# Kernel optimization log

Measured on AMD Instinct MI355X. Metric: run time of the kernel, lower is better.

Reference implementation:

```python
import jax, jax.numpy as jnp
import numpy as np

B = 65536
L, R, D, C = 4, 8, 16, 4
M = D * C          # 64 = d_s2*C
D_S1C = 32         # d_s1*C
OUT = 8


def setup_inputs() -> dict:
    key = jax.random.key(0)
    ks = jax.random.split(key, 16)
    inp = {
        'x': jax.random.uniform(ks[0], (B, 8), dtype=jnp.float32),
        'H': jax.random.normal(ks[1], (B, L, R, D, C), dtype=jnp.float32) * 0.1,
        # VNNILinear / Linear params (not quantized by default -> plain F.linear)
        'W_bit': jax.random.normal(ks[2], (D_S1C, 8), dtype=jnp.float32) * 0.02,
        'b_bit': jnp.zeros((D_S1C,), jnp.float32),
        'W_bridge': jax.random.normal(ks[3], (M, D_S1C), dtype=jnp.float32) * 0.02,
        'W_read': jax.random.normal(ks[4], (OUT, R * M), dtype=jnp.float32) * 0.02,
        'b_read': jnp.zeros((OUT,), jnp.float32),
        # Governor
        'W_sh': jax.random.normal(ks[5], (64, M), dtype=jnp.float32) * 0.02,
        'b_sh': jnp.zeros((64,), jnp.float32),
        'W_eng': jax.random.normal(ks[6], (1, 64), dtype=jnp.float32) * 0.02,
        'b_eng': jnp.zeros((1,), jnp.float32),
        'W_imp': jax.random.normal(ks[7], (1, 64), dtype=jnp.float32) * 0.02,
        'b_imp': jnp.zeros((1,), jnp.float32),
        # surprise heads
        'W_sur': jax.random.normal(ks[8], (1, D_S1C), dtype=jnp.float32) * 0.02,
        'b_sur': jnp.zeros((1,), jnp.float32),
        'W_gate': jax.random.normal(ks[9], (1, D_S1C), dtype=jnp.float32) * 0.02,
        'b_gate': jnp.zeros((1,), jnp.float32),
        # stacked per-slot params
        'decays': jnp.zeros((L, R, M), jnp.float32),
        'halt_w': jax.random.normal(ks[10], (L, R, M), dtype=jnp.float32) * 0.01,
        'halt_b': jnp.zeros((L,), jnp.float32),
    }
    return inp


def reference(x, H, W_bit, b_bit, W_bridge, W_read, b_read, W_sh, b_sh,
              W_eng, b_eng, W_imp, b_imp, W_sur, b_sur, W_gate, b_gate,
              decays, halt_w, halt_b):
    # bit -> s1 latent
    s1 = x @ W_bit.T + b_bit                                   # [B, 32]
    surprise = (jax.nn.sigmoid(s1 @ W_sur.T + b_sur) *
                jax.nn.sigmoid(s1 @ W_gate.T + b_gate))        # [B, 1]
    # bridge to working space
    s2 = jnp.tanh(s1 @ W_bridge.T)                             # [B, 64]
    # governor gates
    hg = jax.nn.relu(s2 @ W_sh.T + b_sh)                       # [B, 64]
    eng = jax.nn.sigmoid(hg @ W_eng.T + b_eng)                 # [B, 1]
    imp = jax.nn.sigmoid(hg @ W_imp.T + b_imp)                 # [B, 1]
    # per-(L,R)-slot halting gate
    halt = jax.nn.sigmoid(jnp.einsum('bm,lrm->blr', s2, halt_w)
                          + halt_b[:, None])                   # [B, L, R]
    gate = halt * (eng * imp)[:, :, None]                      # [B, L, R]
    # gated decay + write into memory slab
    decay_g = jax.nn.sigmoid(decays)                           # [L, R, M]
    Hf = H.reshape(H.shape[0], L, R, M)                        # [B, L, R, M]
    write = (surprise * s2)[:, None, None, :]                  # [B, 1, 1, M]
    H_new = Hf * decay_g[None] + gate[..., None] * write       # [B, L, R, M]
    # read: mean over layers, flatten slots, quantizable readout
    read = H_new.mean(axis=1).reshape(H.shape[0], R * M)       # [B, 512]
    out = read @ W_read.T + b_read                             # [B, 8]
    return out
```

## Files before the change

kernel.cpp:

```cpp
#include <hip/hip_runtime.h>

__device__ __forceinline__ float sigf(float v) {
    return 1.0f / (1.0f + __expf(-v));
}
__device__ __forceinline__ float tanh_fast(float v) {
    return 1.0f - 2.0f / (__expf(2.0f * v) + 1.0f);
}

__global__ __launch_bounds__(64)
void organism_main(const float* __restrict__ x,
                   const float* __restrict__ H,
                   const float* __restrict__ W_bit,
                   const float* __restrict__ b_bit,
                   const float* __restrict__ W_bridge,
                   const float* __restrict__ W_read,
                   const float* __restrict__ b_read,
                   const float* __restrict__ W_sh,
                   const float* __restrict__ b_sh,
                   const float* __restrict__ W_eng,
                   const float* __restrict__ b_eng,
                   const float* __restrict__ W_imp,
                   const float* __restrict__ b_imp,
                   const float* __restrict__ W_sur,
                   const float* __restrict__ b_sur,
                   const float* __restrict__ W_gate,
                   const float* __restrict__ b_gate,
                   const float* __restrict__ decays,
                   const float* __restrict__ halt_w,
                   const float* __restrict__ halt_b,
                   float* __restrict__ out)
{
    const int lane = threadIdx.x;
    const int w    = blockIdx.x;
    const int NW   = gridDim.x;
    const size_t arow = (size_t)w + (size_t)(lane & 31) * NW;

    const float* __restrict__ Hl = H + (size_t)w * 2048 + lane * 4;
    float4 h[8];
#pragma unroll
    for (int it = 0; it < 8; ++it)
        h[it] = *(const float4*)(Hl + it * 256);

    float o2[8];
    {
        float xv[8];
        const float4 x0 = *(const float4*)(x + arow * 8);
        const float4 x1 = *(const float4*)(x + arow * 8 + 4);
        xv[0]=x0.x; xv[1]=x0.y; xv[2]=x0.z; xv[3]=x0.w;
        xv[4]=x1.x; xv[5]=x1.y; xv[6]=x1.z; xv[7]=x1.w;

        float s1[32];
#pragma unroll
        for (int i = 0; i < 32; ++i) {
            float a = b_bit[i];
#pragma unroll
            for (int k = 0; k < 8; ++k) a += W_bit[i*8+k] * xv[k];
            s1[i] = a;
        }

        float sa = b_sur[0], ga = b_gate[0];
#pragma unroll
        for (int i = 0; i < 32; ++i) {
            sa += W_sur[i]  * s1[i];
            ga += W_gate[i] * s1[i];
        }
        const float sur = sigf(sa) * sigf(ga);

        float s2[64];
#pragma unroll
        for (int m = 0; m < 64; ++m) {
            float a = 0.0f;
#pragma unroll
            for (int i = 0; i < 32; ++i) a += W_bridge[m*32+i] * s1[i];
            s2[m] = tanh_fast(a);
        }

        float ea = b_eng[0], ia = b_imp[0];
        for (int n = 0; n < 64; ++n) {
            float a = b_sh[n];
#pragma unroll
            for (int m = 0; m < 64; ++m) a += W_sh[n*64+m] * s2[m];
            a = fmaxf(a, 0.0f);
            ea += W_eng[n] * a;
            ia += W_imp[n] * a;
        }
        const float ei = sigf(ea) * sigf(ia);

        float wv[64];
#pragma unroll
        for (int m = 0; m < 64; ++m) wv[m] = sur * s2[m];

#pragma unroll
        for (int o = 0; o < 8; ++o) o2[o] = b_read[o];
        for (int r = 0; r < 8; ++r) {
            float hs = 0.0f;
#pragma unroll
            for (int l = 0; l < 4; ++l) {
                float a = halt_b[l];
#pragma unroll
                for (int m = 0; m < 64; ++m) a += halt_w[(l*8+r)*64+m] * s2[m];
                hs += sigf(a);
            }
            const float gr = 0.25f * ei * hs;
#pragma unroll
            for (int o = 0; o < 8; ++o) {
                float p = 0.0f;
#pragma unroll
                for (int m = 0; m < 64; ++m) p += W_read[o*512 + r*64 + m] * wv[m];
                o2[o] += gr * p;
            }
        }
    }

    float sd[4][8];
#pragma unroll
    for (int l = 0; l < 4; ++l)
#pragma unroll
        for (int hf = 0; hf < 2; ++hf) {
            const float4 d = *(const float4*)(decays + l*512 + hf*256 + lane*4);
            sd[l][hf*4+0] = 0.25f * sigf(d.x);
            sd[l][hf*4+1] = 0.25f * sigf(d.y);
            sd[l][hf*4+2] = 0.25f * sigf(d.z);
            sd[l][hf*4+3] = 0.25f * sigf(d.w);
        }
    float wrv[8][8];
#pragma unroll
    for (int o = 0; o < 8; ++o)
#pragma unroll
        for (int hf = 0; hf < 2; ++hf) {
            const float4 wq = *(const float4*)(W_read + o*512 + hf*256 + lane*4);
            wrv[o][hf*4+0] = wq.x;
            wrv[o][hf*4+1] = wq.y;
            wrv[o][hf*4+2] = wq.z;
            wrv[o][hf*4+3] = wq.w;
        }

#pragma unroll 1
    for (int rr = 0; rr < 32; ++rr) {
        float g[8];
#pragma unroll
        for (int hf = 0; hf < 2; ++hf) {
            g[hf*4+0] = sd[0][hf*4+0]*h[hf].x   + sd[1][hf*4+0]*h[2+hf].x
                      + sd[2][hf*4+0]*h[4+hf].x + sd[3][hf*4+0]*h[6+hf].x;
            g[hf*4+1] = sd[0][hf*4+1]*h[hf].y   + sd[1][hf*4+1]*h[2+hf].y
                      + sd[2][hf*4+1]*h[4+hf].y + sd[3][hf*4+1]*h[6+hf].y;
            g[hf*4+2] = sd[0][hf*4+2]*h[hf].z   + sd[1][hf*4+2]*h[2+hf].z
                      + sd[2][hf*4+2]*h[4+hf].z + sd[3][hf*4+2]*h[6+hf].z;
            g[hf*4+3] = sd[0][hf*4+3]*h[hf].w   + sd[1][hf*4+3]*h[2+hf].w
                      + sd[2][hf*4+3]*h[4+hf].w + sd[3][hf*4+3]*h[6+hf].w;
        }

        {
            const int nrr = (rr + 1) & 31;
            const float* __restrict__ nb =
                H + ((size_t)w + (size_t)nrr * NW) * 2048 + lane * 4;
#pragma unroll
            for (int it = 0; it < 8; ++it)
                h[it] = *(const float4*)(nb + it * 256);
        }

        float acc[8];
#pragma unroll
        for (int o = 0; o < 8; ++o) {
            float a = 0.0f;
#pragma unroll
            for (int s = 0; s < 8; ++s) a += wrv[o][s] * g[s];
            acc[o] = a;
        }

#pragma unroll
        for (int m = 1; m <= 32; m <<= 1) {
#pragma unroll
            for (int o = 0; o < 8; ++o)
                acc[o] += __shfl_xor(acc[o], m, 64);
        }

        if (lane == rr) {
            float4 a0, a1;
            a0.x = acc[0] + o2[0]; a0.y = acc[1] + o2[1];
            a0.z = acc[2] + o2[2]; a0.w = acc[3] + o2[3];
            a1.x = acc[4] + o2[4]; a1.y = acc[5] + o2[5];
            a1.z = acc[6] + o2[6]; a1.w = acc[7] + o2[7];
            float* op = out + ((size_t)w + (size_t)rr * NW) * 8;
            *(float4*)(op)     = a0;
            *(float4*)(op + 4) = a1;
        }
    }
}

extern "C" void kernel_launch(void* const* d_in, const int* in_sizes, int n_in,
                              void* d_out, int out_size, void* d_ws, size_t ws_size,
                              hipStream_t stream) {
    (void)n_in; (void)d_ws; (void)ws_size; (void)out_size;
    const float* x        = (const float*)d_in[0];
    const float* H        = (const float*)d_in[1];
    const float* W_bit    = (const float*)d_in[2];
    const float* b_bit    = (const float*)d_in[3];
    const float* W_bridge = (const float*)d_in[4];
    const float* W_read   = (const float*)d_in[5];
    const float* b_read   = (const float*)d_in[6];
    const float* W_sh     = (const float*)d_in[7];
    const float* b_sh     = (const float*)d_in[8];
    const float* W_eng    = (const float*)d_in[9];
    const float* b_eng    = (const float*)d_in[10];
    const float* W_imp    = (const float*)d_in[11];
    const float* b_imp    = (const float*)d_in[12];
    const float* W_sur    = (const float*)d_in[13];
    const float* b_sur    = (const float*)d_in[14];
    const float* W_gate   = (const float*)d_in[15];
    const float* b_gate   = (const float*)d_in[16];
    const float* decays   = (const float*)d_in[17];
    const float* halt_w   = (const float*)d_in[18];
    const float* halt_b   = (const float*)d_in[19];
    float* out = (float*)d_out;

    const int B = in_sizes[1] / 2048;
    hipLaunchKernelGGL(organism_main, dim3(B / 32), dim3(64), 0, stream,
                       x, H, W_bit, b_bit, W_bridge, W_read, b_read,
                       W_sh, b_sh, W_eng, b_eng, W_imp, b_imp,
                       W_sur, b_sur, W_gate, b_gate, decays, halt_w, halt_b,
                       out);
}
```

Baseline: 884.2 us.

## Split per-row MLP and H streaming across waves with LDS handoff

Blocks now hold 256 threads covering 64 contiguous rows. Wave 0 computes the per-row MLP for all 64 rows, one row per lane, which removes the old duplication where lanes 32-63 recomputed the same rows. It passes the partial outputs to the other waves through LDS, and all four waves then stream 16 rows of H each. The surprise factor is also folded into a scalar, so the wv array goes away. The cost is that waves 1-3 sit idle at the barrier during the MLP, and the tighter launch bounds may cause register spills.

```diff
diff --git a/kernel.cpp b/kernel.cpp
--- a/kernel.cpp
+++ b/kernel.cpp
@@ -7,7 +7,7 @@
     return 1.0f - 2.0f / (__expf(2.0f * v) + 1.0f);
 }
 
-__global__ __launch_bounds__(64)
+__global__ __launch_bounds__(256, 4)
 void organism_main(const float* __restrict__ x,
                    const float* __restrict__ H,
                    const float* __restrict__ W_bit,
@@ -30,19 +30,15 @@
                    const float* __restrict__ halt_b,
                    float* __restrict__ out)
 {
-    const int lane = threadIdx.x;
-    const int w    = blockIdx.x;
-    const int NW   = gridDim.x;
-    const size_t arow = (size_t)w + (size_t)(lane & 31) * NW;
-
-    const float* __restrict__ Hl = H + (size_t)w * 2048 + lane * 4;
-    float4 h[8];
-#pragma unroll
-    for (int it = 0; it < 8; ++it)
-        h[it] = *(const float4*)(Hl + it * 256);
-
-    float o2[8];
-    {
+    const int tid  = threadIdx.x;
+    const int wave = tid >> 6;
+    const int lane = tid & 63;
+    const size_t rowblk = (size_t)blockIdx.x * 64;
+
+    __shared__ float o2_lds[64][8];
+
+    if (wave == 0) {
+        const size_t arow = rowblk + lane;
         float xv[8];
         const float4 x0 = *(const float4*)(x + arow * 8);
         const float4 x1 = *(const float4*)(x + arow * 8 + 4);
@@ -84,12 +80,9 @@
             ea += W_eng[n] * a;
             ia += W_imp[n] * a;
         }
-        const float ei = sigf(ea) * sigf(ia);
-
-        float wv[64];
-#pragma unroll
-        for (int m = 0; m < 64; ++m) wv[m] = sur * s2[m];
-
+        const float eis = 0.25f * sigf(ea) * sigf(ia) * sur;
+
+        float o2[8];
 #pragma unroll
         for (int o = 0; o < 8; ++o) o2[o] = b_read[o];
         for (int r = 0; r < 8; ++r) {
@@ -101,15 +94,17 @@
                 for (int m = 0; m < 64; ++m) a += halt_w[(l*8+r)*64+m] * s2[m];
                 hs += sigf(a);
             }
-            const float gr = 0.25f * ei * hs;
+            const float grs = eis * hs;
 #pragma unroll
             for (int o = 0; o < 8; ++o) {
                 float p = 0.0f;
 #pragma unroll
-                for (int m = 0; m < 64; ++m) p += W_read[o*512 + r*64 + m] * wv[m];
-                o2[o] += gr * p;
+                for (int m = 0; m < 64; ++m) p += W_read[o*512 + r*64 + m] * s2[m];
+                o2[o] += grs * p;
             }
         }
+        *(float4*)&o2_lds[lane][0] = make_float4(o2[0], o2[1], o2[2], o2[3]);
+        *(float4*)&o2_lds[lane][4] = make_float4(o2[4], o2[5], o2[6], o2[7]);
     }
 
     float sd[4][8];
@@ -135,8 +130,17 @@
             wrv[o][hf*4+3] = wq.w;
         }
 
+    const size_t wrow0 = rowblk + (size_t)wave * 16;
+    const float* __restrict__ Hl = H + wrow0 * 2048 + lane * 4;
+    float4 h[8];
+#pragma unroll
+    for (int it = 0; it < 8; ++it)
+        h[it] = *(const float4*)(Hl + it * 256);
+
+    __syncthreads();
+
 #pragma unroll 1
-    for (int rr = 0; rr < 32; ++rr) {
+    for (int rr = 0; rr < 16; ++rr) {
         float g[8];
 #pragma unroll
         for (int hf = 0; hf < 2; ++hf) {
@@ -151,9 +155,8 @@
         }
 
         {
-            const int nrr = (rr + 1) & 31;
-            const float* __restrict__ nb =
-                H + ((size_t)w + (size_t)nrr * NW) * 2048 + lane * 4;
+            const int nrr = (rr + 1) & 15;
+            const float* __restrict__ nb = H + (wrow0 + nrr) * 2048 + lane * 4;
 #pragma unroll
             for (int it = 0; it < 8; ++it)
                 h[it] = *(const float4*)(nb + it * 256);
@@ -176,12 +179,15 @@
         }
 
         if (lane == rr) {
+            const int lrow = wave * 16 + rr;
+            const float4 oA = *(const float4*)&o2_lds[lrow][0];
+            const float4 oB = *(const float4*)&o2_lds[lrow][4];
             float4 a0, a1;
-            a0.x = acc[0] + o2[0]; a0.y = acc[1] + o2[1];
-            a0.z = acc[2] + o2[2]; a0.w = acc[3] + o2[3];
-            a1.x = acc[4] + o2[4]; a1.y = acc[5] + o2[5];
-            a1.z = acc[6] + o2[6]; a1.w = acc[7] + o2[7];
-            float* op = out + ((size_t)w + (size_t)rr * NW) * 8;
+            a0.x = acc[0] + oA.x; a0.y = acc[1] + oA.y;
+            a0.z = acc[2] + oA.z; a0.w = acc[3] + oA.w;
+            a1.x = acc[4] + oB.x; a1.y = acc[5] + oB.y;
+            a1.z = acc[6] + oB.z; a1.w = acc[7] + oB.w;
+            float* op = out + (rowblk + lrow) * 8;
             *(float4*)(op)     = a0;
             *(float4*)(op + 4) = a1;
         }
@@ -215,7 +221,7 @@
     float* out = (float*)d_out;
 
     const int B = in_sizes[1] / 2048;
-    hipLaunchKernelGGL(organism_main, dim3(B / 32), dim3(64), 0, stream,
+    hipLaunchKernelGGL(organism_main, dim3(B / 64), dim3(256), 0, stream,
                        x, H, W_bit, b_bit, W_bridge, W_read, b_read,
                        W_sh, b_sh, W_eng, b_eng, W_imp, b_imp,
                        W_sur, b_sur, W_gate, b_gate, decays, halt_w, halt_b,
```

Result: slower. 1.675 ms (+89.4%).
